# Performance work log

Hardware: AMD Instinct MI355X
Metric: run time of the kernel (lower is better)

Reference implementation:

```python
import jax, jax.numpy as jnp
import numpy as np

NUM_TOKENS = 65536
D_MODEL = 2048
NUM_EXPERTS = 64


def setup_inputs() -> dict:
    key = jax.random.key(0)
    kx, kw = jax.random.split(key)
    x = jax.random.normal(kx, (NUM_TOKENS, D_MODEL), dtype=jnp.float32)
    W = jax.random.normal(kw, (NUM_EXPERTS, D_MODEL), dtype=jnp.float32) * (1.0 / np.sqrt(D_MODEL))
    return {"x": x, "W": W}


def reference(x, W):
    # logits = x @ W^T : [T, E]
    logits = jnp.einsum("td,ed->te", x, W)
    probs = jax.nn.softmax(logits, axis=-1)
    top_idx = jnp.argmax(probs, axis=-1)                     # [T]
    expert_indices = jax.nn.one_hot(top_idx, NUM_EXPERTS, dtype=jnp.int32)  # [T, E]
    top_prob = jnp.max(probs, axis=-1, keepdims=True)        # [T, 1]
    return expert_indices, top_prob, logits
```

## Files before the change

### kernel.cpp

```cpp
#include <hip/hip_runtime.h>


constexpr int T_TOK = 65536;
constexpr int DM    = 2048;
constexpr int NE    = 64;
constexpr int BM    = 128;
constexpr int BK    = 64;
constexpr int PR    = 68;

__global__ __launch_bounds__(256, 2)
void router_kernel(const float* __restrict__ x, const float* __restrict__ W,
                   float* __restrict__ onehot, float* __restrict__ topp,
                   float* __restrict__ logits)
{
    __shared__ float xs[BM][PR];
    __shared__ float ws[BK][PR];

    const int tid = threadIdx.x;
    const int tx  = tid & 15;
    const int ty  = tid >> 4;
    const long t0 = (long)blockIdx.x * BM;

    float acc[8][4];
#pragma unroll
    for (int i = 0; i < 8; ++i)
#pragma unroll
        for (int j = 0; j < 4; ++j) acc[i][j] = 0.0f;

    const int s_tok = tid >> 4;
    const int s_k   = (tid & 15) * 4;

    for (int kc = 0; kc < DM; kc += BK) {
        if (kc) __syncthreads();

#pragma unroll
        for (int p = 0; p < 8; ++p) {
            const int t = p * 16 + s_tok;
            const float4 v = *(const float4*)(x + (t0 + t) * DM + kc + s_k);
            *(float4*)(&xs[t][s_k]) = v;
        }
#pragma unroll
        for (int p = 0; p < 4; ++p) {
            const int e = p * 16 + s_tok;
            const float4 v = *(const float4*)(W + (long)e * DM + kc + s_k);
            ws[s_k + 0][e] = v.x;
            ws[s_k + 1][e] = v.y;
            ws[s_k + 2][e] = v.z;
            ws[s_k + 3][e] = v.w;
        }
        __syncthreads();

#pragma unroll
        for (int kk = 0; kk < BK; kk += 4) {
            float wv[4][4];
#pragma unroll
            for (int dk = 0; dk < 4; ++dk)
                *(float4*)wv[dk] = *(const float4*)(&ws[kk + dk][tx * 4]);
#pragma unroll
            for (int i = 0; i < 8; ++i) {
                const float4 xv = *(const float4*)(&xs[ty + 16 * i][kk]);
                float xa[4] = {xv.x, xv.y, xv.z, xv.w};
#pragma unroll
                for (int j = 0; j < 4; ++j) {
#pragma unroll
                    for (int dk = 0; dk < 4; ++dk)
                        acc[i][j] = fmaf(xa[dk], wv[dk][j], acc[i][j]);
                }
            }
        }
    }

#pragma unroll
    for (int i = 0; i < 8; ++i) {
        const long tok = t0 + ty + 16 * i;

        float m  = acc[i][0];
        int   mi = tx * 4;
#pragma unroll
        for (int j = 1; j < 4; ++j) {
            if (acc[i][j] > m) { m = acc[i][j]; mi = tx * 4 + j; }
        }
#pragma unroll
        for (int d = 1; d < 16; d <<= 1) {
            const float om  = __shfl_xor(m, d, 64);
            const int   omi = __shfl_xor(mi, d, 64);
            if (om > m || (om == m && omi < mi)) { m = om; mi = omi; }
        }
        float s = 0.0f;
#pragma unroll
        for (int j = 0; j < 4; ++j) s += __expf(acc[i][j] - m);
#pragma unroll
        for (int d = 1; d < 16; d <<= 1) s += __shfl_xor(s, d, 64);

        float4 oh, lg;
        oh.x = (tx * 4 + 0 == mi) ? 1.0f : 0.0f;
        oh.y = (tx * 4 + 1 == mi) ? 1.0f : 0.0f;
        oh.z = (tx * 4 + 2 == mi) ? 1.0f : 0.0f;
        oh.w = (tx * 4 + 3 == mi) ? 1.0f : 0.0f;
        lg.x = acc[i][0]; lg.y = acc[i][1]; lg.z = acc[i][2]; lg.w = acc[i][3];

        *(float4*)(onehot + tok * NE + tx * 4) = oh;
        *(float4*)(logits + tok * NE + tx * 4) = lg;
        if (tx == 0) topp[tok] = 1.0f / s;
    }
}

extern "C" void kernel_launch(void* const* d_in, const int* in_sizes, int n_in,
                              void* d_out, int out_size, void* d_ws, size_t ws_size,
                              hipStream_t stream)
{
    const float* x = (const float*)d_in[0];
    const float* W = (const float*)d_in[1];
    float* out = (float*)d_out;

    float* onehot = out;
    float* topp   = out + (long)T_TOK * NE;
    float* logits = topp + T_TOK;

    router_kernel<<<dim3(T_TOK / BM), dim3(256), 0, stream>>>(x, W, onehot, topp, logits);
}
```

Before: 795.3 us.

## Replace FP32 FMA GEMM with split-bf16x3 MFMA and register-prefetched double buffering

Replaces the scalar FP32 FMA tiling with bf16 MFMA 16x16x32 instructions. Each FP32 value is split into three bf16 terms and six cross products are accumulated to approximate FP32 precision. x fragments stay in registers, W is split once per chunk into double-buffered LDS, and the next chunk's global loads are issued before the current MFMAs run. The aim is to move the compute-bound dot products onto matrix cores, at the cost of extra split ALU work and scalar output stores.

After: 729.1 us. -8.3%, faster.

```diff
diff --git a/kernel.cpp b/kernel.cpp
--- a/kernel.cpp
+++ b/kernel.cpp
@@ -6,102 +6,188 @@
 constexpr int NE    = 64;
 constexpr int BM    = 128;
 constexpr int BK    = 64;
-constexpr int PR    = 68;
+constexpr int NCH   = DM / BK;
+constexpr int WPAD  = 72;
+constexpr int PLANE = NE * WPAD;
+constexpr int WBUF  = 3 * PLANE;
+
+typedef __attribute__((ext_vector_type(8))) short bf16x8;
+typedef __attribute__((ext_vector_type(4))) float f32x4;
+
+__device__ __forceinline__ void split3(const f32x4& a, const f32x4& b,
+                                       bf16x8& h, bf16x8& m, bf16x8& l) {
+#pragma unroll
+    for (int j = 0; j < 8; ++j) {
+        const float xv = (j < 4) ? a[j] : b[j - 4];
+        const unsigned u0 = __float_as_uint(xv);
+        h[j] = (short)(u0 >> 16);
+        const float r1 = xv - __uint_as_float(u0 & 0xFFFF0000u);
+        const unsigned u1 = __float_as_uint(r1);
+        m[j] = (short)(u1 >> 16);
+        const float r2 = r1 - __uint_as_float(u1 & 0xFFFF0000u);
+        l[j] = (short)(__float_as_uint(r2) >> 16);
+    }
+}
 
 __global__ __launch_bounds__(256, 2)
-void router_kernel(const float* __restrict__ x, const float* __restrict__ W,
-                   float* __restrict__ onehot, float* __restrict__ topp,
-                   float* __restrict__ logits)
+void router_mfma(const float* __restrict__ x, const float* __restrict__ W,
+                 float* __restrict__ onehot, float* __restrict__ topp,
+                 float* __restrict__ logits)
 {
-    __shared__ float xs[BM][PR];
-    __shared__ float ws[BK][PR];
-
-    const int tid = threadIdx.x;
-    const int tx  = tid & 15;
-    const int ty  = tid >> 4;
-    const long t0 = (long)blockIdx.x * BM;
-
-    float acc[8][4];
-#pragma unroll
-    for (int i = 0; i < 8; ++i)
-#pragma unroll
-        for (int j = 0; j < 4; ++j) acc[i][j] = 0.0f;
-
-    const int s_tok = tid >> 4;
-    const int s_k   = (tid & 15) * 4;
-
-    for (int kc = 0; kc < DM; kc += BK) {
-        if (kc) __syncthreads();
-
-#pragma unroll
-        for (int p = 0; p < 8; ++p) {
-            const int t = p * 16 + s_tok;
-            const float4 v = *(const float4*)(x + (t0 + t) * DM + kc + s_k);
-            *(float4*)(&xs[t][s_k]) = v;
-        }
-#pragma unroll
-        for (int p = 0; p < 4; ++p) {
-            const int e = p * 16 + s_tok;
-            const float4 v = *(const float4*)(W + (long)e * DM + kc + s_k);
-            ws[s_k + 0][e] = v.x;
-            ws[s_k + 1][e] = v.y;
-            ws[s_k + 2][e] = v.z;
-            ws[s_k + 3][e] = v.w;
+    __shared__ __align__(16) unsigned short wlds[2 * WBUF];
+
+    const int tid  = threadIdx.x;
+    const int lane = tid & 63;
+    const int wave = tid >> 6;
+    const int r16  = lane & 15;
+    const int quad = lane >> 4;
+
+    const long blk_t0 = (long)blockIdx.x * BM;
+    const long trow0  = blk_t0 + wave * 32 + r16;
+    const long trow1  = trow0 + 16;
+
+    const float* xp0 = x + trow0 * DM + quad * 8;
+    const float* xp1 = x + trow1 * DM + quad * 8;
+
+    const int we  = tid >> 2;
+    const int wk0 = (tid & 3) * 16;
+    const float* wp = W + (long)we * DM + wk0;
+    const int wo = we * WPAD + wk0;
+
+    f32x4 acc[2][4];
+#pragma unroll
+    for (int mt = 0; mt < 2; ++mt)
+#pragma unroll
+        for (int nt = 0; nt < 4; ++nt) acc[mt][nt] = (f32x4){0.f, 0.f, 0.f, 0.f};
+
+    f32x4 xn[2][2][2];
+    f32x4 wn[4];
+    bf16x8 af[2][2][3];
+
+#pragma unroll
+    for (int mt = 0; mt < 2; ++mt)
+#pragma unroll
+        for (int ks = 0; ks < 2; ++ks) {
+            const float* p = (mt ? xp1 : xp0) + ks * 32;
+            xn[mt][ks][0] = *(const f32x4*)p;
+            xn[mt][ks][1] = *(const f32x4*)(p + 4);
+        }
+#pragma unroll
+    for (int j = 0; j < 4; ++j) wn[j] = *(const f32x4*)(wp + j * 4);
+
+#pragma unroll
+    for (int mt = 0; mt < 2; ++mt)
+#pragma unroll
+        for (int ks = 0; ks < 2; ++ks)
+            split3(xn[mt][ks][0], xn[mt][ks][1],
+                   af[mt][ks][0], af[mt][ks][1], af[mt][ks][2]);
+    {
+        bf16x8 h0, m0, l0, h1, m1, l1;
+        split3(wn[0], wn[1], h0, m0, l0);
+        split3(wn[2], wn[3], h1, m1, l1);
+        unsigned short* wb = wlds;
+        *(bf16x8*)(wb + 0 * PLANE + wo)     = h0;
+        *(bf16x8*)(wb + 0 * PLANE + wo + 8) = h1;
+        *(bf16x8*)(wb + 1 * PLANE + wo)     = m0;
+        *(bf16x8*)(wb + 1 * PLANE + wo + 8) = m1;
+        *(bf16x8*)(wb + 2 * PLANE + wo)     = l0;
+        *(bf16x8*)(wb + 2 * PLANE + wo + 8) = l1;
+    }
+    __syncthreads();
+
+    for (int kc = 0; kc < NCH; ++kc) {
+        const int nxt = kc + 1;
+        if (nxt < NCH) {
+#pragma unroll
+            for (int mt = 0; mt < 2; ++mt)
+#pragma unroll
+                for (int ks = 0; ks < 2; ++ks) {
+                    const float* p = (mt ? xp1 : xp0) + nxt * BK + ks * 32;
+                    xn[mt][ks][0] = *(const f32x4*)p;
+                    xn[mt][ks][1] = *(const f32x4*)(p + 4);
+                }
+#pragma unroll
+            for (int j = 0; j < 4; ++j) wn[j] = *(const f32x4*)(wp + nxt * BK + j * 4);
+        }
+
+        const unsigned short* wb = wlds + (kc & 1) * WBUF;
+        const int bo = r16 * WPAD + quad * 8;
+#pragma unroll
+        for (int ks = 0; ks < 2; ++ks) {
+#pragma unroll
+            for (int nt = 0; nt < 4; ++nt) {
+                const int eo = (nt * 16) * WPAD + bo + ks * 32;
+                const bf16x8 bh = *(const bf16x8*)(wb + 0 * PLANE + eo);
+                const bf16x8 bm = *(const bf16x8*)(wb + 1 * PLANE + eo);
+                const bf16x8 bl = *(const bf16x8*)(wb + 2 * PLANE + eo);
+#pragma unroll
+                for (int mt = 0; mt < 2; ++mt) {
+                    f32x4 c = acc[mt][nt];
+                    c = __builtin_amdgcn_mfma_f32_16x16x32_bf16(af[mt][ks][0], bh, c, 0, 0, 0);
+                    c = __builtin_amdgcn_mfma_f32_16x16x32_bf16(af[mt][ks][1], bh, c, 0, 0, 0);
+                    c = __builtin_amdgcn_mfma_f32_16x16x32_bf16(af[mt][ks][2], bh, c, 0, 0, 0);
+                    c = __builtin_amdgcn_mfma_f32_16x16x32_bf16(af[mt][ks][0], bm, c, 0, 0, 0);
+                    c = __builtin_amdgcn_mfma_f32_16x16x32_bf16(af[mt][ks][1], bm, c, 0, 0, 0);
+                    c = __builtin_amdgcn_mfma_f32_16x16x32_bf16(af[mt][ks][0], bl, c, 0, 0, 0);
+                    acc[mt][nt] = c;
+                }
+            }
+        }
+
+        if (nxt < NCH) {
+#pragma unroll
+            for (int mt = 0; mt < 2; ++mt)
+#pragma unroll
+                for (int ks = 0; ks < 2; ++ks)
+                    split3(xn[mt][ks][0], xn[mt][ks][1],
+                           af[mt][ks][0], af[mt][ks][1], af[mt][ks][2]);
+            bf16x8 h0, m0, l0, h1, m1, l1;
+            split3(wn[0], wn[1], h0, m0, l0);
+            split3(wn[2], wn[3], h1, m1, l1);
+            unsigned short* wb2 = wlds + (nxt & 1) * WBUF;
+            *(bf16x8*)(wb2 + 0 * PLANE + wo)     = h0;
+            *(bf16x8*)(wb2 + 0 * PLANE + wo + 8) = h1;
+            *(bf16x8*)(wb2 + 1 * PLANE + wo)     = m0;
+            *(bf16x8*)(wb2 + 1 * PLANE + wo + 8) = m1;
+            *(bf16x8*)(wb2 + 2 * PLANE + wo)     = l0;
+            *(bf16x8*)(wb2 + 2 * PLANE + wo + 8) = l1;
         }
         __syncthreads();
-
-#pragma unroll
-        for (int kk = 0; kk < BK; kk += 4) {
-            float wv[4][4];
-#pragma unroll
-            for (int dk = 0; dk < 4; ++dk)
-                *(float4*)wv[dk] = *(const float4*)(&ws[kk + dk][tx * 4]);
-#pragma unroll
-            for (int i = 0; i < 8; ++i) {
-                const float4 xv = *(const float4*)(&xs[ty + 16 * i][kk]);
-                float xa[4] = {xv.x, xv.y, xv.z, xv.w};
-#pragma unroll
-                for (int j = 0; j < 4; ++j) {
-#pragma unroll
-                    for (int dk = 0; dk < 4; ++dk)
-                        acc[i][j] = fmaf(xa[dk], wv[dk][j], acc[i][j]);
-                }
-            }
-        }
-    }
-
-#pragma unroll
-    for (int i = 0; i < 8; ++i) {
-        const long tok = t0 + ty + 16 * i;
-
-        float m  = acc[i][0];
-        int   mi = tx * 4;
-#pragma unroll
-        for (int j = 1; j < 4; ++j) {
-            if (acc[i][j] > m) { m = acc[i][j]; mi = tx * 4 + j; }
-        }
-#pragma unroll
-        for (int d = 1; d < 16; d <<= 1) {
-            const float om  = __shfl_xor(m, d, 64);
-            const int   omi = __shfl_xor(mi, d, 64);
-            if (om > m || (om == m && omi < mi)) { m = om; mi = omi; }
-        }
-        float s = 0.0f;
-#pragma unroll
-        for (int j = 0; j < 4; ++j) s += __expf(acc[i][j] - m);
-#pragma unroll
-        for (int d = 1; d < 16; d <<= 1) s += __shfl_xor(s, d, 64);
-
-        float4 oh, lg;
-        oh.x = (tx * 4 + 0 == mi) ? 1.0f : 0.0f;
-        oh.y = (tx * 4 + 1 == mi) ? 1.0f : 0.0f;
-        oh.z = (tx * 4 + 2 == mi) ? 1.0f : 0.0f;
-        oh.w = (tx * 4 + 3 == mi) ? 1.0f : 0.0f;
-        lg.x = acc[i][0]; lg.y = acc[i][1]; lg.z = acc[i][2]; lg.w = acc[i][3];
-
-        *(float4*)(onehot + tok * NE + tx * 4) = oh;
-        *(float4*)(logits + tok * NE + tx * 4) = lg;
-        if (tx == 0) topp[tok] = 1.0f / s;
+    }
+
+#pragma unroll
+    for (int mt = 0; mt < 2; ++mt) {
+#pragma unroll
+        for (int reg = 0; reg < 4; ++reg) {
+            const long t = blk_t0 + wave * 32 + mt * 16 + quad * 4 + reg;
+
+            float mval = acc[mt][0][reg];
+            int   mi   = r16;
+#pragma unroll
+            for (int nt = 1; nt < 4; ++nt) {
+                const float v = acc[mt][nt][reg];
+                if (v > mval) { mval = v; mi = nt * 16 + r16; }
+            }
+#pragma unroll
+            for (int d = 1; d < 16; d <<= 1) {
+                const float om = __shfl_xor(mval, d, 64);
+                const int   oi = __shfl_xor(mi, d, 64);
+                if (om > mval || (om == mval && oi < mi)) { mval = om; mi = oi; }
+            }
+            float s = 0.f;
+#pragma unroll
+            for (int nt = 0; nt < 4; ++nt) s += __expf(acc[mt][nt][reg] - mval);
+#pragma unroll
+            for (int d = 1; d < 16; d <<= 1) s += __shfl_xor(s, d, 64);
+
+            const long ob = t * NE + r16;
+#pragma unroll
+            for (int nt = 0; nt < 4; ++nt) {
+                logits[ob + nt * 16] = acc[mt][nt][reg];
+                onehot[ob + nt * 16] = (nt * 16 + r16 == mi) ? 1.0f : 0.0f;
+            }
+            if (r16 == 0) topp[t] = 1.0f / s;
+        }
     }
 }
 
@@ -117,5 +203,5 @@
     float* topp   = out + (long)T_TOK * NE;
     float* logits = topp + T_TOK;
 
-    router_kernel<<<dim3(T_TOK / BM), dim3(256), 0, stream>>>(x, W, onehot, topp, logits);
+    router_mfma<<<dim3(T_TOK / BM), dim3(256), 0, stream>>>(x, W, onehot, topp, logits);
 }
```
